# Performance work log

Hardware: AMD Instinct MI355X
Metric: run time of the kernel (lower is better)

The kernel has to match this reference:

```python
import jax, jax.numpy as jnp
import numpy as np
from jax import lax

NUM_CLASSES = 4   # includes ignore label 0
IGNORE = 0
MAX_SAMPLES = 1024
HALF = MAX_SAMPLES // 2
BIG = 1 << 30     # sentinel key for invalid/unselected pixels


def setup_inputs() -> dict:
    key = jax.random.key(0)
    k1, k2, k3 = jax.random.split(key, 3)
    B, C, H, W = 4, 64, 256, 256
    feat_map = jax.random.normal(k1, (B, C, H, W), dtype=jnp.float32)
    labels = jax.random.randint(k2, (B, H, W), 0, NUM_CLASSES, dtype=jnp.int32)
    preds = jax.random.normal(k3, (B, NUM_CLASSES, H, W), dtype=jnp.float32)
    return {"feat_map": feat_map, "labels": labels, "preds": preds}


def _soft_dilate2d(x):
    # F.max_pool2d(x, kernel=3, stride=1, padding=1) on [B,1,H,W]
    return lax.reduce_window(x, -jnp.inf, lax.max, (1, 1, 3, 3), (1, 1, 1, 1), "SAME")


def _per_pair(fm, lab, pd, cls):
    # fm: [C, N] features, lab: [N] int labels, pd: [N] dilated pred class, cls: scalar int
    N = lab.shape[0]
    ar = jnp.arange(N)
    clsf = cls.astype(pd.dtype)
    in_cls = lab == cls
    hard = (pd != clsf) & in_cls   # mispredicted (after dilation) pixels of this class
    easy = (pd == clsf) & in_cls
    # torch code uses randperm; reference uses the deterministic identity
    # permutation: keep the first HALF hard pixels (in raster order).
    hard_key = jnp.where(hard, ar, BIG)
    hard_top = jnp.sort(hard_key)[:HALF]                      # [HALF]
    valid_h = (hard_top < BIG).astype(fm.dtype)
    feat_h = fm[:, jnp.where(hard_top < BIG, hard_top, 0)] * valid_h  # [C, HALF], zero-padded
    # rest pool = leftover hard pixels (rank >= HALF) first, then easy pixels;
    # keep first HALF of that concatenation.
    hard_rank = jnp.cumsum(hard) - 1
    easy_rank = jnp.cumsum(easy) - 1
    excess = jnp.maximum(jnp.sum(hard) - HALF, 0)
    rest_key = jnp.where(hard & (hard_rank >= HALF), hard_rank - HALF,
                         jnp.where(easy, excess + easy_rank, BIG))
    order = jnp.argsort(rest_key)[:HALF]                      # pixel indices, valid first
    valid_r = (jnp.take(rest_key, order) < BIG).astype(fm.dtype)
    feat_r = fm[:, order] * valid_r                           # [C, HALF], zero-padded
    return jnp.concatenate([feat_h, feat_r], axis=1)          # [C, MAX_SAMPLES]


def reference(feat_map, labels, preds):
    B, C, H, W = feat_map.shape
    N = H * W
    # softmax preserves argmax -> skip the softmax
    pred_lab = jnp.argmax(preds, axis=1).astype(feat_map.dtype)[:, None]  # [B,1,H,W]
    preds_d = _soft_dilate2d(pred_lab).reshape(B, N)
    feat_flat = feat_map.reshape(B, C, N)
    lab_flat = labels.reshape(B, N)
    # assume all non-ignore classes present in each image (true w.h.p. for
    # random labels over 65536 pixels) -> static total_classes = B*(NUM_CLASSES-1)
    b_idx = jnp.repeat(jnp.arange(B), NUM_CLASSES - 1)
    cls_idx = jnp.tile(jnp.arange(1, NUM_CLASSES), B)
    feat_extract = jax.vmap(_per_pair)(feat_flat[b_idx], lab_flat[b_idx],
                                       preds_d[b_idx], cls_idx)  # [B*(NC-1), C, 1024]
    feat_label = cls_idx.astype(jnp.float32)
    return feat_extract, feat_label
```

## Files before the change

### kernel.cpp

```cpp
#include <hip/hip_runtime.h>

#define BB 4
#define CC 64
#define HH 256
#define WW 256
#define NPIX (HH*WW)
#define NCLS 4
#define NPAIR 12
#define HALF 512
#define MAXS 1024
#define NOUT (NPAIR*CC*MAXS)
#define CHUNK 4096
#define NCHUNK (NPIX/CHUNK)

__global__ void k_dargmax(const float* __restrict__ preds, unsigned char* __restrict__ pd) {
    __shared__ unsigned char am[6][WW];
    __shared__ unsigned char vm[4][WW];
    int b = blockIdx.y;
    int y0 = blockIdx.x * 4;
    int x = threadIdx.x;
    const float* pb = preds + (size_t)b * NCLS * NPIX;
#pragma unroll
    for (int r = 0; r < 6; ++r) {
        int y = y0 + r - 1;
        unsigned char a = 0;
        if (y >= 0 && y < HH) {
            const float* p = pb + y * WW + x;
            float best = p[0];
            int arg = 0;
#pragma unroll
            for (int c = 1; c < NCLS; ++c) {
                float v = p[(size_t)c * NPIX];
                if (v > best) { best = v; arg = c; }
            }
            a = (unsigned char)arg;
        }
        am[r][x] = a;
    }
    __syncthreads();
#pragma unroll
    for (int ry = 0; ry < 4; ++ry) {
        int m = am[ry][x];
        int v1 = am[ry + 1][x], v2 = am[ry + 2][x];
        if (v1 > m) m = v1;
        if (v2 > m) m = v2;
        vm[ry][x] = (unsigned char)m;
    }
    __syncthreads();
#pragma unroll
    for (int ry = 0; ry < 4; ++ry) {
        int m = vm[ry][x];
        if (x > 0)      { int v = vm[ry][x - 1]; if (v > m) m = v; }
        if (x < WW - 1) { int v = vm[ry][x + 1]; if (v > m) m = v; }
        pd[b * NPIX + (y0 + ry) * WW + x] = (unsigned char)m;
    }
}

__global__ void k_count(const int* __restrict__ labels, const unsigned char* __restrict__ pd,
                        unsigned* __restrict__ chunkCounts, int* __restrict__ slots) {
    int chunk = blockIdx.x, b = blockIdx.y, t = threadIdx.x;
    int gid = (b * NCHUNK + chunk) * 256 + t;
    if (gid < NPAIR * MAXS) slots[gid] = -1;

    const int4*   lab4 = (const int4*)(labels + b * NPIX);
    const uchar4* pd4  = (const uchar4*)(pd + b * NPIX);
    unsigned pk[3] = {0u, 0u, 0u};
#pragma unroll
    for (int j = 0; j < 4; ++j) {
        int idx = chunk * (CHUNK / 4) + j * 256 + t;
        int4 lv = lab4[idx];
        uchar4 dv = pd4[idx];
        int ls[4] = {lv.x, lv.y, lv.z, lv.w};
        int ds[4] = {dv.x, dv.y, dv.z, dv.w};
#pragma unroll
        for (int e = 0; e < 4; ++e) {
#pragma unroll
            for (int c = 0; c < 3; ++c) {
                if (ls[e] == c + 1) pk[c] += (ds[e] == c + 1) ? (1u << 16) : 1u;
            }
        }
    }
    int lane = t & 63, w = t >> 6;
#pragma unroll
    for (int c = 0; c < 3; ++c)
#pragma unroll
        for (int off = 32; off > 0; off >>= 1)
            pk[c] += (unsigned)__shfl_down((int)pk[c], off, 64);
    __shared__ unsigned ws[4][3];
    if (lane == 0) { ws[w][0] = pk[0]; ws[w][1] = pk[1]; ws[w][2] = pk[2]; }
    __syncthreads();
    if (t < 3)
        chunkCounts[(b * 3 + t) * NCHUNK + chunk] =
            ws[0][t] + ws[1][t] + ws[2][t] + ws[3][t];
}

__global__ void k_scan(const unsigned* __restrict__ chunkCounts, int2* __restrict__ chunkBases,
                       int* __restrict__ excessArr, float* __restrict__ out) {
    int t = threadIdx.x;
    if (t < NPAIR) {
        int hb = 0, eb = 0;
        for (int ch = 0; ch < NCHUNK; ++ch) {
            unsigned v = chunkCounts[t * NCHUNK + ch];
            chunkBases[t * NCHUNK + ch] = make_int2(hb, eb);
            hb += (int)(v & 0xffffu);
            eb += (int)(v >> 16);
        }
        int ex = hb - HALF;
        excessArr[t] = ex > 0 ? ex : 0;
        out[NOUT + t] = (float)(t % 3 + 1);
    }
}

__global__ void k_assign(const int* __restrict__ labels, const unsigned char* __restrict__ pd,
                         const int2* __restrict__ chunkBases, const int* __restrict__ excessArr,
                         int* __restrict__ slots) {
    int chunk = blockIdx.x, pair = blockIdx.y, t = threadIdx.x;
    int b = pair / 3, cls = pair % 3 + 1;
    int2 base = chunkBases[pair * NCHUNK + chunk];
    int excess = excessArr[pair];
    if (base.x >= MAXS && HALF + excess + base.y >= MAXS) return;

    const int4* lab4 = (const int4*)(labels + b * NPIX + chunk * CHUNK + t * 16);
    const uint4* pd16 = (const uint4*)(pd + b * NPIX + chunk * CHUNK + t * 16);
    int4 l0 = lab4[0], l1 = lab4[1], l2 = lab4[2], l3 = lab4[3];
    uint4 dp = pd16[0];
    int ls[16] = {l0.x, l0.y, l0.z, l0.w, l1.x, l1.y, l1.z, l1.w,
                  l2.x, l2.y, l2.z, l2.w, l3.x, l3.y, l3.z, l3.w};
    unsigned char ds[16];
    unsigned dw[4] = {dp.x, dp.y, dp.z, dp.w};
#pragma unroll
    for (int j = 0; j < 16; ++j) ds[j] = (dw[j >> 2] >> ((j & 3) * 8)) & 0xff;

    unsigned mine = 0;
#pragma unroll
    for (int j = 0; j < 16; ++j)
        if (ls[j] == cls) mine += (ds[j] == cls) ? (1u << 16) : 1u;

    int lane = t & 63, w = t >> 6;
    unsigned v = mine;
#pragma unroll
    for (int off = 1; off < 64; off <<= 1) {
        unsigned u = (unsigned)__shfl_up((int)v, off, 64);
        if (lane >= off) v += u;
    }
    __shared__ unsigned ws[4];
    if (lane == 63) ws[w] = v;
    __syncthreads();
    unsigned waveBase = 0;
    for (int i = 0; i < w; ++i) waveBase += ws[i];
    unsigned excl = waveBase + v - mine;

    int hr = base.x + (int)(excl & 0xffffu);
    int er = base.y + (int)(excl >> 16);
    int pixBase = chunk * CHUNK + t * 16;
    int* sl = slots + pair * MAXS;
#pragma unroll
    for (int j = 0; j < 16; ++j) {
        if (ls[j] == cls) {
            if (ds[j] != cls) {
                if (hr < MAXS) sl[hr] = pixBase + j;
                hr++;
            } else {
                int pos = HALF + excess + er;
                if (pos < MAXS) sl[pos] = pixBase + j;
                er++;
            }
        }
    }
}

__global__ void k_gather(const float* __restrict__ feat, const int* __restrict__ slots,
                         float* __restrict__ out) {
    int i = blockIdx.x * blockDim.x + threadIdx.x;
    const int NQ = NOUT / 4;
    if (i >= NQ) return;
    int q = i << 2;
    int pair = q >> 16;
    int c = (q >> 10) & (CC - 1);
    int slot = q & (MAXS - 1);
    int b = pair / 3;
    const float* fp = feat + ((size_t)(b * CC + c)) * NPIX;
    const int* sp = slots + pair * MAXS + slot;
    int p0 = sp[0], p1 = sp[1], p2 = sp[2], p3 = sp[3];
    float4 o;
    o.x = (p0 >= 0) ? fp[p0] : 0.0f;
    o.y = (p1 >= 0) ? fp[p1] : 0.0f;
    o.z = (p2 >= 0) ? fp[p2] : 0.0f;
    o.w = (p3 >= 0) ? fp[p3] : 0.0f;
    ((float4*)out)[i] = o;
}

extern "C" void kernel_launch(void* const* d_in, const int* in_sizes, int n_in,
                              void* d_out, int out_size, void* d_ws, size_t ws_size,
                              hipStream_t stream) {
    const float* feat   = (const float*)d_in[0];
    const int*   labels = (const int*)d_in[1];
    const float* preds  = (const float*)d_in[2];
    float* out = (float*)d_out;

    unsigned char* pd = (unsigned char*)d_ws;
    int* slots = (int*)(pd + BB * NPIX);
    int2* chunkBases = (int2*)(slots + NPAIR * MAXS);
    unsigned* chunkCounts = (unsigned*)(chunkBases + NPAIR * NCHUNK);
    int* excessArr = (int*)(chunkCounts + NPAIR * NCHUNK);

    k_dargmax<<<dim3(HH / 4, BB), 256, 0, stream>>>(preds, pd);
    k_count<<<dim3(NCHUNK, BB), 256, 0, stream>>>(labels, pd, chunkCounts, slots);
    k_scan<<<1, 64, 0, stream>>>(chunkCounts, chunkBases, excessArr, out);
    k_assign<<<dim3(NCHUNK, NPAIR), 256, 0, stream>>>(labels, pd, chunkBases, excessArr, slots);
    k_gather<<<(NOUT / 4 + 255) / 256, 256, 0, stream>>>(feat, slots, out);
}
```

Before: 109.5 us.

## Fuse five pipeline kernels into one cooperative kernel with grid syncs

Merges the dilated-argmax, count, scan, assign and gather kernels into a single cooperative launch of 256 blocks separated by grid-wide barriers. This removes four kernel launch boundaries and their inter-kernel gaps. In exchange, the gather stage now runs on a fixed 256-block grid with three iterations per thread instead of a large grid, and grid.sync costs plus idle blocks in the small count and scan phases add serialization.

```diff
diff --git a/kernel.cpp b/kernel.cpp
--- a/kernel.cpp
+++ b/kernel.cpp
@@ -1,4 +1,7 @@
 #include <hip/hip_runtime.h>
+#include <hip/hip_cooperative_groups.h>
+
+namespace cg = cooperative_groups;
 
 #define BB 4
 #define CC 64
@@ -13,91 +16,96 @@
 #define CHUNK 4096
 #define NCHUNK (NPIX/CHUNK)
 
-__global__ void k_dargmax(const float* __restrict__ preds, unsigned char* __restrict__ pd) {
+__global__ void __launch_bounds__(256) k_fused(
+        const float* __restrict__ feat, const int* __restrict__ labels,
+        const float* __restrict__ preds, float* __restrict__ out,
+        unsigned char* __restrict__ pd, int* __restrict__ slots,
+        int2* __restrict__ chunkBases, unsigned* __restrict__ chunkCounts,
+        int* __restrict__ excessArr) {
+    cg::grid_group grid = cg::this_grid();
+    int bx = blockIdx.x, t = threadIdx.x;
+
     __shared__ unsigned char am[6][WW];
     __shared__ unsigned char vm[4][WW];
-    int b = blockIdx.y;
-    int y0 = blockIdx.x * 4;
-    int x = threadIdx.x;
-    const float* pb = preds + (size_t)b * NCLS * NPIX;
-#pragma unroll
-    for (int r = 0; r < 6; ++r) {
-        int y = y0 + r - 1;
-        unsigned char a = 0;
-        if (y >= 0 && y < HH) {
-            const float* p = pb + y * WW + x;
-            float best = p[0];
-            int arg = 0;
-#pragma unroll
-            for (int c = 1; c < NCLS; ++c) {
-                float v = p[(size_t)c * NPIX];
-                if (v > best) { best = v; arg = c; }
+    __shared__ unsigned ws3[4][3];
+    __shared__ unsigned ws4[4];
+
+    {
+        int b = bx >> 6;
+        int y0 = (bx & 63) * 4;
+        int x = t;
+        const float* pb = preds + (size_t)b * NCLS * NPIX;
+#pragma unroll
+        for (int r = 0; r < 6; ++r) {
+            int y = y0 + r - 1;
+            unsigned char a = 0;
+            if (y >= 0 && y < HH) {
+                const float* p = pb + y * WW + x;
+                float best = p[0];
+                int arg = 0;
+#pragma unroll
+                for (int c = 1; c < NCLS; ++c) {
+                    float v = p[(size_t)c * NPIX];
+                    if (v > best) { best = v; arg = c; }
+                }
+                a = (unsigned char)arg;
             }
-            a = (unsigned char)arg;
-        }
-        am[r][x] = a;
-    }
-    __syncthreads();
-#pragma unroll
-    for (int ry = 0; ry < 4; ++ry) {
-        int m = am[ry][x];
-        int v1 = am[ry + 1][x], v2 = am[ry + 2][x];
-        if (v1 > m) m = v1;
-        if (v2 > m) m = v2;
-        vm[ry][x] = (unsigned char)m;
-    }
-    __syncthreads();
-#pragma unroll
-    for (int ry = 0; ry < 4; ++ry) {
-        int m = vm[ry][x];
-        if (x > 0)      { int v = vm[ry][x - 1]; if (v > m) m = v; }
-        if (x < WW - 1) { int v = vm[ry][x + 1]; if (v > m) m = v; }
-        pd[b * NPIX + (y0 + ry) * WW + x] = (unsigned char)m;
-    }
-}
-
-__global__ void k_count(const int* __restrict__ labels, const unsigned char* __restrict__ pd,
-                        unsigned* __restrict__ chunkCounts, int* __restrict__ slots) {
-    int chunk = blockIdx.x, b = blockIdx.y, t = threadIdx.x;
-    int gid = (b * NCHUNK + chunk) * 256 + t;
-    if (gid < NPAIR * MAXS) slots[gid] = -1;
-
-    const int4*   lab4 = (const int4*)(labels + b * NPIX);
-    const uchar4* pd4  = (const uchar4*)(pd + b * NPIX);
-    unsigned pk[3] = {0u, 0u, 0u};
-#pragma unroll
-    for (int j = 0; j < 4; ++j) {
-        int idx = chunk * (CHUNK / 4) + j * 256 + t;
-        int4 lv = lab4[idx];
-        uchar4 dv = pd4[idx];
-        int ls[4] = {lv.x, lv.y, lv.z, lv.w};
-        int ds[4] = {dv.x, dv.y, dv.z, dv.w};
-#pragma unroll
-        for (int e = 0; e < 4; ++e) {
-#pragma unroll
-            for (int c = 0; c < 3; ++c) {
-                if (ls[e] == c + 1) pk[c] += (ds[e] == c + 1) ? (1u << 16) : 1u;
-            }
-        }
-    }
-    int lane = t & 63, w = t >> 6;
-#pragma unroll
-    for (int c = 0; c < 3; ++c)
-#pragma unroll
-        for (int off = 32; off > 0; off >>= 1)
-            pk[c] += (unsigned)__shfl_down((int)pk[c], off, 64);
-    __shared__ unsigned ws[4][3];
-    if (lane == 0) { ws[w][0] = pk[0]; ws[w][1] = pk[1]; ws[w][2] = pk[2]; }
-    __syncthreads();
-    if (t < 3)
-        chunkCounts[(b * 3 + t) * NCHUNK + chunk] =
-            ws[0][t] + ws[1][t] + ws[2][t] + ws[3][t];
-}
-
-__global__ void k_scan(const unsigned* __restrict__ chunkCounts, int2* __restrict__ chunkBases,
-                       int* __restrict__ excessArr, float* __restrict__ out) {
-    int t = threadIdx.x;
-    if (t < NPAIR) {
+            am[r][x] = a;
+        }
+        __syncthreads();
+#pragma unroll
+        for (int ry = 0; ry < 4; ++ry) {
+            int m = am[ry][x];
+            int v1 = am[ry + 1][x], v2 = am[ry + 2][x];
+            if (v1 > m) m = v1;
+            if (v2 > m) m = v2;
+            vm[ry][x] = (unsigned char)m;
+        }
+        __syncthreads();
+#pragma unroll
+        for (int ry = 0; ry < 4; ++ry) {
+            int m = vm[ry][x];
+            if (x > 0)      { int v = vm[ry][x - 1]; if (v > m) m = v; }
+            if (x < WW - 1) { int v = vm[ry][x + 1]; if (v > m) m = v; }
+            pd[b * NPIX + (y0 + ry) * WW + x] = (unsigned char)m;
+        }
+    }
+    grid.sync();
+
+    if (bx < 48) slots[bx * 256 + t] = -1;
+    if (bx < 64) {
+        int chunk = bx & 15, b = bx >> 4;
+        const int4*   lab4 = (const int4*)(labels + b * NPIX);
+        const uchar4* pd4  = (const uchar4*)(pd + b * NPIX);
+        unsigned pk[3] = {0u, 0u, 0u};
+#pragma unroll
+        for (int j = 0; j < 4; ++j) {
+            int idx = chunk * (CHUNK / 4) + j * 256 + t;
+            int4 lv = lab4[idx];
+            uchar4 dv = pd4[idx];
+            int ls[4] = {lv.x, lv.y, lv.z, lv.w};
+            int ds[4] = {dv.x, dv.y, dv.z, dv.w};
+#pragma unroll
+            for (int e = 0; e < 4; ++e)
+#pragma unroll
+                for (int c = 0; c < 3; ++c)
+                    if (ls[e] == c + 1) pk[c] += (ds[e] == c + 1) ? (1u << 16) : 1u;
+        }
+        int lane = t & 63, w = t >> 6;
+#pragma unroll
+        for (int c = 0; c < 3; ++c)
+#pragma unroll
+            for (int off = 32; off > 0; off >>= 1)
+                pk[c] += (unsigned)__shfl_down((int)pk[c], off, 64);
+        if (lane == 0) { ws3[w][0] = pk[0]; ws3[w][1] = pk[1]; ws3[w][2] = pk[2]; }
+        __syncthreads();
+        if (t < 3)
+            chunkCounts[(b * 3 + t) * NCHUNK + chunk] =
+                ws3[0][t] + ws3[1][t] + ws3[2][t] + ws3[3][t];
+    }
+    grid.sync();
+
+    if (bx == 0 && t < NPAIR) {
         int hb = 0, eb = 0;
         for (int ch = 0; ch < NCHUNK; ++ch) {
             unsigned v = chunkCounts[t * NCHUNK + ch];
@@ -109,85 +117,85 @@
         excessArr[t] = ex > 0 ? ex : 0;
         out[NOUT + t] = (float)(t % 3 + 1);
     }
-}
-
-__global__ void k_assign(const int* __restrict__ labels, const unsigned char* __restrict__ pd,
-                         const int2* __restrict__ chunkBases, const int* __restrict__ excessArr,
-                         int* __restrict__ slots) {
-    int chunk = blockIdx.x, pair = blockIdx.y, t = threadIdx.x;
-    int b = pair / 3, cls = pair % 3 + 1;
-    int2 base = chunkBases[pair * NCHUNK + chunk];
-    int excess = excessArr[pair];
-    if (base.x >= MAXS && HALF + excess + base.y >= MAXS) return;
-
-    const int4* lab4 = (const int4*)(labels + b * NPIX + chunk * CHUNK + t * 16);
-    const uint4* pd16 = (const uint4*)(pd + b * NPIX + chunk * CHUNK + t * 16);
-    int4 l0 = lab4[0], l1 = lab4[1], l2 = lab4[2], l3 = lab4[3];
-    uint4 dp = pd16[0];
-    int ls[16] = {l0.x, l0.y, l0.z, l0.w, l1.x, l1.y, l1.z, l1.w,
-                  l2.x, l2.y, l2.z, l2.w, l3.x, l3.y, l3.z, l3.w};
-    unsigned char ds[16];
-    unsigned dw[4] = {dp.x, dp.y, dp.z, dp.w};
-#pragma unroll
-    for (int j = 0; j < 16; ++j) ds[j] = (dw[j >> 2] >> ((j & 3) * 8)) & 0xff;
-
-    unsigned mine = 0;
-#pragma unroll
-    for (int j = 0; j < 16; ++j)
-        if (ls[j] == cls) mine += (ds[j] == cls) ? (1u << 16) : 1u;
-
-    int lane = t & 63, w = t >> 6;
-    unsigned v = mine;
-#pragma unroll
-    for (int off = 1; off < 64; off <<= 1) {
-        unsigned u = (unsigned)__shfl_up((int)v, off, 64);
-        if (lane >= off) v += u;
-    }
-    __shared__ unsigned ws[4];
-    if (lane == 63) ws[w] = v;
-    __syncthreads();
-    unsigned waveBase = 0;
-    for (int i = 0; i < w; ++i) waveBase += ws[i];
-    unsigned excl = waveBase + v - mine;
-
-    int hr = base.x + (int)(excl & 0xffffu);
-    int er = base.y + (int)(excl >> 16);
-    int pixBase = chunk * CHUNK + t * 16;
-    int* sl = slots + pair * MAXS;
-#pragma unroll
-    for (int j = 0; j < 16; ++j) {
-        if (ls[j] == cls) {
-            if (ds[j] != cls) {
-                if (hr < MAXS) sl[hr] = pixBase + j;
-                hr++;
-            } else {
-                int pos = HALF + excess + er;
-                if (pos < MAXS) sl[pos] = pixBase + j;
-                er++;
+    grid.sync();
+
+    if (bx < NPAIR * NCHUNK) {
+        int pair = bx >> 4, chunk = bx & 15;
+        int b = pair / 3, cls = pair % 3 + 1;
+        int2 base = chunkBases[pair * NCHUNK + chunk];
+        int excess = excessArr[pair];
+        if (!(base.x >= MAXS && HALF + excess + base.y >= MAXS)) {
+            const int4* lab4 = (const int4*)(labels + b * NPIX + chunk * CHUNK + t * 16);
+            const uint4* pd16 = (const uint4*)(pd + b * NPIX + chunk * CHUNK + t * 16);
+            int4 l0 = lab4[0], l1 = lab4[1], l2 = lab4[2], l3 = lab4[3];
+            uint4 dp = pd16[0];
+            int ls[16] = {l0.x, l0.y, l0.z, l0.w, l1.x, l1.y, l1.z, l1.w,
+                          l2.x, l2.y, l2.z, l2.w, l3.x, l3.y, l3.z, l3.w};
+            unsigned char ds[16];
+            unsigned dw[4] = {dp.x, dp.y, dp.z, dp.w};
+#pragma unroll
+            for (int j = 0; j < 16; ++j) ds[j] = (dw[j >> 2] >> ((j & 3) * 8)) & 0xff;
+
+            unsigned mine = 0;
+#pragma unroll
+            for (int j = 0; j < 16; ++j)
+                if (ls[j] == cls) mine += (ds[j] == cls) ? (1u << 16) : 1u;
+
+            int lane = t & 63, w = t >> 6;
+            unsigned v = mine;
+#pragma unroll
+            for (int off = 1; off < 64; off <<= 1) {
+                unsigned u = (unsigned)__shfl_up((int)v, off, 64);
+                if (lane >= off) v += u;
             }
-        }
-    }
-}
-
-__global__ void k_gather(const float* __restrict__ feat, const int* __restrict__ slots,
-                         float* __restrict__ out) {
-    int i = blockIdx.x * blockDim.x + threadIdx.x;
-    const int NQ = NOUT / 4;
-    if (i >= NQ) return;
-    int q = i << 2;
-    int pair = q >> 16;
-    int c = (q >> 10) & (CC - 1);
-    int slot = q & (MAXS - 1);
-    int b = pair / 3;
-    const float* fp = feat + ((size_t)(b * CC + c)) * NPIX;
-    const int* sp = slots + pair * MAXS + slot;
-    int p0 = sp[0], p1 = sp[1], p2 = sp[2], p3 = sp[3];
-    float4 o;
-    o.x = (p0 >= 0) ? fp[p0] : 0.0f;
-    o.y = (p1 >= 0) ? fp[p1] : 0.0f;
-    o.z = (p2 >= 0) ? fp[p2] : 0.0f;
-    o.w = (p3 >= 0) ? fp[p3] : 0.0f;
-    ((float4*)out)[i] = o;
+            if (lane == 63) ws4[w] = v;
+            __syncthreads();
+            unsigned waveBase = 0;
+            for (int i = 0; i < w; ++i) waveBase += ws4[i];
+            unsigned excl = waveBase + v - mine;
+
+            int hr = base.x + (int)(excl & 0xffffu);
+            int er = base.y + (int)(excl >> 16);
+            int pixBase = chunk * CHUNK + t * 16;
+            int* sl = slots + pair * MAXS;
+#pragma unroll
+            for (int j = 0; j < 16; ++j) {
+                if (ls[j] == cls) {
+                    if (ds[j] != cls) {
+                        if (hr < MAXS) sl[hr] = pixBase + j;
+                        hr++;
+                    } else {
+                        int pos = HALF + excess + er;
+                        if (pos < MAXS) sl[pos] = pixBase + j;
+                        er++;
+                    }
+                }
+            }
+        }
+    }
+    grid.sync();
+
+    {
+        int i0 = bx * 256 + t;
+#pragma unroll
+        for (int k = 0; k < 3; ++k) {
+            int i = i0 + k * 65536;
+            int q = i << 2;
+            int pair = q >> 16;
+            int c = (q >> 10) & (CC - 1);
+            int slot = q & (MAXS - 1);
+            int b = pair / 3;
+            const float* fp = feat + ((size_t)(b * CC + c)) * NPIX;
+            const int* sp = slots + pair * MAXS + slot;
+            int p0 = sp[0], p1 = sp[1], p2 = sp[2], p3 = sp[3];
+            float4 o;
+            o.x = (p0 >= 0) ? fp[p0] : 0.0f;
+            o.y = (p1 >= 0) ? fp[p1] : 0.0f;
+            o.z = (p2 >= 0) ? fp[p2] : 0.0f;
+            o.w = (p3 >= 0) ? fp[p3] : 0.0f;
+            ((float4*)out)[i] = o;
+        }
+    }
 }
 
 extern "C" void kernel_launch(void* const* d_in, const int* in_sizes, int n_in,
@@ -204,9 +212,8 @@
     unsigned* chunkCounts = (unsigned*)(chunkBases + NPAIR * NCHUNK);
     int* excessArr = (int*)(chunkCounts + NPAIR * NCHUNK);
 
-    k_dargmax<<<dim3(HH / 4, BB), 256, 0, stream>>>(preds, pd);
-    k_count<<<dim3(NCHUNK, BB), 256, 0, stream>>>(labels, pd, chunkCounts, slots);
-    k_scan<<<1, 64, 0, stream>>>(chunkCounts, chunkBases, excessArr, out);
-    k_assign<<<dim3(NCHUNK, NPAIR), 256, 0, stream>>>(labels, pd, chunkBases, excessArr, slots);
-    k_gather<<<(NOUT / 4 + 255) / 256, 256, 0, stream>>>(feat, slots, out);
+    void* args[] = {(void*)&feat, (void*)&labels, (void*)&preds, (void*)&out,
+                    (void*)&pd, (void*)&slots, (void*)&chunkBases,
+                    (void*)&chunkCounts, (void*)&excessArr};
+    hipLaunchCooperativeKernel((void*)k_fused, dim3(256), dim3(256), args, 0, stream);
 }
```

After: 221.2 us. +102.1%, slower.

## Fuse counting into dilated-argmax kernel and fold scan into assign

Applied to the files above, without the earlier changes.

Per-band class counting moves into the dilated-argmax kernel, and each assign block computes its own chunk prefix from the band counts, which removes the separate count and scan kernels. Five launches become three. Slot validity in the gather is now derived from the per-pair totals instead of a -1 sentinel, so the slot buffer no longer needs initialising. In exchange, each assign block redundantly sums 64 band counts, and the vertical argmax window is kept in registers rather than shared memory.

```diff
diff --git a/kernel.cpp b/kernel.cpp
--- a/kernel.cpp
+++ b/kernel.cpp
@@ -12,14 +12,21 @@
 #define NOUT (NPAIR*CC*MAXS)
 #define CHUNK 4096
 #define NCHUNK (NPIX/CHUNK)
-
-__global__ void k_dargmax(const float* __restrict__ preds, unsigned char* __restrict__ pd) {
-    __shared__ unsigned char am[6][WW];
+#define NBAND 64
+#define BANDPIX (NPIX/NBAND)
+
+__global__ void __launch_bounds__(256) k_dargmax(
+        const float* __restrict__ preds, const int* __restrict__ labels,
+        unsigned char* __restrict__ pd, unsigned* __restrict__ bandCounts) {
     __shared__ unsigned char vm[4][WW];
-    int b = blockIdx.y;
-    int y0 = blockIdx.x * 4;
+    __shared__ unsigned wsum[4][3];
+    int bx = blockIdx.x;
+    int b = bx >> 6, band = bx & 63;
+    int y0 = band * 4;
     int x = threadIdx.x;
     const float* pb = preds + (size_t)b * NCLS * NPIX;
+
+    unsigned char am[6];
 #pragma unroll
     for (int r = 0; r < 6; ++r) {
         int y = y0 + r - 1;
@@ -35,90 +42,72 @@
             }
             a = (unsigned char)arg;
         }
-        am[r][x] = a;
-    }
-    __syncthreads();
+        am[r] = a;
+    }
+    unsigned char vmr[4];
 #pragma unroll
     for (int ry = 0; ry < 4; ++ry) {
-        int m = am[ry][x];
-        int v1 = am[ry + 1][x], v2 = am[ry + 2][x];
-        if (v1 > m) m = v1;
-        if (v2 > m) m = v2;
+        int m = am[ry];
+        if (am[ry + 1] > m) m = am[ry + 1];
+        if (am[ry + 2] > m) m = am[ry + 2];
+        vmr[ry] = (unsigned char)m;
         vm[ry][x] = (unsigned char)m;
     }
     __syncthreads();
+
+    unsigned pk[3] = {0u, 0u, 0u};
 #pragma unroll
     for (int ry = 0; ry < 4; ++ry) {
-        int m = vm[ry][x];
+        int m = vmr[ry];
         if (x > 0)      { int v = vm[ry][x - 1]; if (v > m) m = v; }
         if (x < WW - 1) { int v = vm[ry][x + 1]; if (v > m) m = v; }
-        pd[b * NPIX + (y0 + ry) * WW + x] = (unsigned char)m;
-    }
-}
-
-__global__ void k_count(const int* __restrict__ labels, const unsigned char* __restrict__ pd,
-                        unsigned* __restrict__ chunkCounts, int* __restrict__ slots) {
-    int chunk = blockIdx.x, b = blockIdx.y, t = threadIdx.x;
-    int gid = (b * NCHUNK + chunk) * 256 + t;
-    if (gid < NPAIR * MAXS) slots[gid] = -1;
-
-    const int4*   lab4 = (const int4*)(labels + b * NPIX);
-    const uchar4* pd4  = (const uchar4*)(pd + b * NPIX);
-    unsigned pk[3] = {0u, 0u, 0u};
-#pragma unroll
-    for (int j = 0; j < 4; ++j) {
-        int idx = chunk * (CHUNK / 4) + j * 256 + t;
-        int4 lv = lab4[idx];
-        uchar4 dv = pd4[idx];
-        int ls[4] = {lv.x, lv.y, lv.z, lv.w};
-        int ds[4] = {dv.x, dv.y, dv.z, dv.w};
-#pragma unroll
-        for (int e = 0; e < 4; ++e) {
-#pragma unroll
-            for (int c = 0; c < 3; ++c) {
-                if (ls[e] == c + 1) pk[c] += (ds[e] == c + 1) ? (1u << 16) : 1u;
-            }
-        }
-    }
-    int lane = t & 63, w = t >> 6;
+        int idx = b * NPIX + (y0 + ry) * WW + x;
+        pd[idx] = (unsigned char)m;
+        int l = labels[idx];
+#pragma unroll
+        for (int c = 0; c < 3; ++c)
+            if (l == c + 1) pk[c] += (m == c + 1) ? (1u << 16) : 1u;
+    }
+    int lane = x & 63, w = x >> 6;
 #pragma unroll
     for (int c = 0; c < 3; ++c)
 #pragma unroll
         for (int off = 32; off > 0; off >>= 1)
             pk[c] += (unsigned)__shfl_down((int)pk[c], off, 64);
-    __shared__ unsigned ws[4][3];
-    if (lane == 0) { ws[w][0] = pk[0]; ws[w][1] = pk[1]; ws[w][2] = pk[2]; }
-    __syncthreads();
-    if (t < 3)
-        chunkCounts[(b * 3 + t) * NCHUNK + chunk] =
-            ws[0][t] + ws[1][t] + ws[2][t] + ws[3][t];
-}
-
-__global__ void k_scan(const unsigned* __restrict__ chunkCounts, int2* __restrict__ chunkBases,
-                       int* __restrict__ excessArr, float* __restrict__ out) {
+    if (lane == 0) { wsum[w][0] = pk[0]; wsum[w][1] = pk[1]; wsum[w][2] = pk[2]; }
+    __syncthreads();
+    if (x < 3)
+        bandCounts[(b * 3 + x) * NBAND + band] =
+            wsum[0][x] + wsum[1][x] + wsum[2][x] + wsum[3][x];
+}
+
+__global__ void __launch_bounds__(256) k_assign(
+        const int* __restrict__ labels, const unsigned char* __restrict__ pd,
+        const unsigned* __restrict__ bandCounts, unsigned* __restrict__ pairTotals,
+        int* __restrict__ slots, float* __restrict__ out) {
+    int pair = blockIdx.x >> 4, chunk = blockIdx.x & 15;
+    int b = pair / 3, cls = pair % 3 + 1;
     int t = threadIdx.x;
-    if (t < NPAIR) {
-        int hb = 0, eb = 0;
-        for (int ch = 0; ch < NCHUNK; ++ch) {
-            unsigned v = chunkCounts[t * NCHUNK + ch];
-            chunkBases[t * NCHUNK + ch] = make_int2(hb, eb);
-            hb += (int)(v & 0xffffu);
-            eb += (int)(v >> 16);
-        }
-        int ex = hb - HALF;
-        excessArr[t] = ex > 0 ? ex : 0;
-        out[NOUT + t] = (float)(t % 3 + 1);
-    }
-}
-
-__global__ void k_assign(const int* __restrict__ labels, const unsigned char* __restrict__ pd,
-                         const int2* __restrict__ chunkBases, const int* __restrict__ excessArr,
-                         int* __restrict__ slots) {
-    int chunk = blockIdx.x, pair = blockIdx.y, t = threadIdx.x;
-    int b = pair / 3, cls = pair % 3 + 1;
-    int2 base = chunkBases[pair * NCHUNK + chunk];
-    int excess = excessArr[pair];
-    if (base.x >= MAXS && HALF + excess + base.y >= MAXS) return;
+    __shared__ unsigned bc[NBAND];
+    __shared__ unsigned ws[4];
+    if (t < NBAND) bc[t] = bandCounts[pair * NBAND + t];
+    __syncthreads();
+    unsigned base = 0, total = 0;
+    int cut = chunk * 4;
+#pragma unroll
+    for (int i = 0; i < NBAND; ++i) {
+        unsigned v = bc[i];
+        total += v;
+        if (i < cut) base += v;
+    }
+    if (chunk == 0 && t == 0) {
+        pairTotals[pair] = total;
+        out[NOUT + pair] = (float)cls;
+    }
+    int excess = (int)(total & 0xffffu) - HALF;
+    if (excess < 0) excess = 0;
+    int baseH = (int)(base & 0xffffu), baseE = (int)(base >> 16);
+    if (baseH >= MAXS && HALF + excess + baseE >= MAXS) return;
 
     const int4* lab4 = (const int4*)(labels + b * NPIX + chunk * CHUNK + t * 16);
     const uint4* pd16 = (const uint4*)(pd + b * NPIX + chunk * CHUNK + t * 16);
@@ -143,15 +132,14 @@
         unsigned u = (unsigned)__shfl_up((int)v, off, 64);
         if (lane >= off) v += u;
     }
-    __shared__ unsigned ws[4];
     if (lane == 63) ws[w] = v;
     __syncthreads();
     unsigned waveBase = 0;
     for (int i = 0; i < w; ++i) waveBase += ws[i];
     unsigned excl = waveBase + v - mine;
 
-    int hr = base.x + (int)(excl & 0xffffu);
-    int er = base.y + (int)(excl >> 16);
+    int hr = baseH + (int)(excl & 0xffffu);
+    int er = baseE + (int)(excl >> 16);
     int pixBase = chunk * CHUNK + t * 16;
     int* sl = slots + pair * MAXS;
 #pragma unroll
@@ -169,25 +157,34 @@
     }
 }
 
-__global__ void k_gather(const float* __restrict__ feat, const int* __restrict__ slots,
-                         float* __restrict__ out) {
-    int i = blockIdx.x * blockDim.x + threadIdx.x;
-    const int NQ = NOUT / 4;
-    if (i >= NQ) return;
+__global__ void __launch_bounds__(256) k_gather(
+        const float* __restrict__ feat, const int* __restrict__ slots,
+        const unsigned* __restrict__ pairTotals, float* __restrict__ out) {
+    int i = blockIdx.x * 256 + threadIdx.x;
     int q = i << 2;
     int pair = q >> 16;
+    unsigned tot = pairTotals[pair];
+    int Nh = (int)(tot & 0xffffu), Ne = (int)(tot >> 16);
+    int excess = Nh - HALF; if (excess < 0) excess = 0;
+    int hardEnd = Nh < MAXS ? Nh : MAXS;
+    int easyStart = HALF + excess;
+    int easyEnd = easyStart + Ne; if (easyEnd > MAXS) easyEnd = MAXS;
+
     int c = (q >> 10) & (CC - 1);
     int slot = q & (MAXS - 1);
     int b = pair / 3;
     const float* fp = feat + ((size_t)(b * CC + c)) * NPIX;
     const int* sp = slots + pair * MAXS + slot;
-    int p0 = sp[0], p1 = sp[1], p2 = sp[2], p3 = sp[3];
-    float4 o;
-    o.x = (p0 >= 0) ? fp[p0] : 0.0f;
-    o.y = (p1 >= 0) ? fp[p1] : 0.0f;
-    o.z = (p2 >= 0) ? fp[p2] : 0.0f;
-    o.w = (p3 >= 0) ? fp[p3] : 0.0f;
-    ((float4*)out)[i] = o;
+    float o[4];
+#pragma unroll
+    for (int j = 0; j < 4; ++j) {
+        int s = slot + j;
+        bool valid = (s < hardEnd) || (s >= easyStart && s < easyEnd);
+        float val = 0.0f;
+        if (valid) val = fp[sp[j]];
+        o[j] = val;
+    }
+    ((float4*)out)[i] = make_float4(o[0], o[1], o[2], o[3]);
 }
 
 extern "C" void kernel_launch(void* const* d_in, const int* in_sizes, int n_in,
@@ -200,13 +197,10 @@
 
     unsigned char* pd = (unsigned char*)d_ws;
     int* slots = (int*)(pd + BB * NPIX);
-    int2* chunkBases = (int2*)(slots + NPAIR * MAXS);
-    unsigned* chunkCounts = (unsigned*)(chunkBases + NPAIR * NCHUNK);
-    int* excessArr = (int*)(chunkCounts + NPAIR * NCHUNK);
-
-    k_dargmax<<<dim3(HH / 4, BB), 256, 0, stream>>>(preds, pd);
-    k_count<<<dim3(NCHUNK, BB), 256, 0, stream>>>(labels, pd, chunkCounts, slots);
-    k_scan<<<1, 64, 0, stream>>>(chunkCounts, chunkBases, excessArr, out);
-    k_assign<<<dim3(NCHUNK, NPAIR), 256, 0, stream>>>(labels, pd, chunkBases, excessArr, slots);
-    k_gather<<<(NOUT / 4 + 255) / 256, 256, 0, stream>>>(feat, slots, out);
-}
+    unsigned* bandCounts = (unsigned*)(slots + NPAIR * MAXS);
+    unsigned* pairTotals = bandCounts + NPAIR * NBAND;
+
+    k_dargmax<<<NBAND * BB, 256, 0, stream>>>(preds, labels, pd, bandCounts);
+    k_assign<<<NPAIR * NCHUNK, 256, 0, stream>>>(labels, pd, bandCounts, pairTotals, slots, out);
+    k_gather<<<NOUT / 4 / 256, 256, 0, stream>>>(feat, slots, pairTotals, out);
+}
```

After: 106.5 us. 2.7% less time.
